# Performance work log

Measured on AMD Instinct MI355X. Metric: run time of the kernel, lower is better.

Reference implementation:

```python
import jax, jax.numpy as jnp
import numpy as np

N_NODES = 50000
N_EDGES = 800000
N_GRAPHS = 64
D_IN = 768
D_HID = 256


def gcn_conv(x, src, dst, W, b, n_nodes):
    """PyG GCNConv: symmetric-normalized aggregation with self-loops.
    out = D^{-1/2} (A + I) D^{-1/2} (x @ W) + b
    """
    h = x @ W  # [N, C_out]
    # degree from target nodes, counting the implicit self-loop (+1)
    deg = jax.ops.segment_sum(jnp.ones((src.shape[0],), h.dtype), dst,
                              num_segments=n_nodes) + 1.0
    dinv = jax.lax.rsqrt(deg)  # deg >= 1 always (self-loop)
    norm = (dinv[src] * dinv[dst])[:, None]  # [E, 1]
    agg = jax.ops.segment_sum(h[src] * norm, dst, num_segments=n_nodes)
    # self-loop contribution: norm_ii = dinv_i^2
    agg = agg + (dinv * dinv)[:, None] * h
    return agg + b


def global_mean_pool(x, batch, n_graphs):
    s = jax.ops.segment_sum(x, batch, num_segments=n_graphs)
    cnt = jax.ops.segment_sum(jnp.ones((x.shape[0],), x.dtype), batch,
                              num_segments=n_graphs)
    return s / jnp.maximum(cnt, 1.0)[:, None]


def setup_inputs() -> dict:
    key = jax.random.key(0)
    ks = jax.random.split(key, 12)
    x = jax.random.normal(ks[0], (N_NODES, D_IN), jnp.float32)
    edge_index = jax.random.randint(ks[1], (2, N_EDGES), 0, N_NODES, jnp.int64)
    batch = jnp.sort(jax.random.randint(ks[2], (N_NODES,), 0, N_GRAPHS, jnp.int64))
    def glorot(k, shape):
        lim = np.sqrt(6.0 / (shape[0] + shape[1]))
        return jax.random.uniform(k, shape, jnp.float32, -lim, lim)
    return {
        "x": x, "edge_index": edge_index, "batch": batch,
        "W1": glorot(ks[3], (D_IN, D_HID)), "b1": jnp.zeros((D_HID,), jnp.float32),
        "W2": glorot(ks[4], (D_HID, D_HID)), "b2": jnp.zeros((D_HID,), jnp.float32),
        "W3": glorot(ks[5], (D_HID, D_HID)), "b3": jnp.zeros((D_HID,), jnp.float32),
        "Wl": glorot(ks[6], (D_HID, D_IN)), "bl": jnp.zeros((D_IN,), jnp.float32),
    }


def reference(x, edge_index, batch, W1, b1, W2, b2, W3, b3, Wl, bl):
    src, dst = edge_index[0], edge_index[1]
    n = x.shape[0]
    # dropout is identity in eval mode
    h = jax.nn.relu(gcn_conv(x, src, dst, W1, b1, n))
    h = jax.nn.relu(gcn_conv(h, src, dst, W2, b2, n))
    h = gcn_conv(h, src, dst, W3, b3, n)
    g = global_mean_pool(h, batch, N_GRAPHS)  # [G, D_HID]
    return g @ Wl + bl  # [G, D_IN]
```

## Files before the change

kernel.cpp:

```cpp
#include <hip/hip_runtime.h>
#include <hip/hip_bf16.h>

#define D_IN 768
#define D_HID 256

typedef __attribute__((ext_vector_type(8))) short short8;
typedef __attribute__((ext_vector_type(4))) float f32x4;

__device__ inline float b2f(unsigned short u) {
    unsigned x = ((unsigned)u) << 16;
    union { unsigned u; float f; } c; c.u = x; return c.f;
}
__device__ inline unsigned short f2b(float v) {
    __hip_bfloat16 h = __float2bfloat16(v);
    return *(unsigned short*)&h;
}

__device__ inline void gload_lds16(const void* g, void* l) {
    __builtin_amdgcn_global_load_lds(
        (const __attribute__((address_space(1))) unsigned int*)g,
        (__attribute__((address_space(3))) unsigned int*)l, 16, 0, 0);
}


__global__ void k_count(const int* __restrict__ dst, int* __restrict__ deg, int E) {
    int i = blockIdx.x * 256 + threadIdx.x;
    if (i < E) atomicAdd(&deg[dst[i]], 1);
}

__global__ void k_dinv(const int* __restrict__ deg, float* __restrict__ dinv, int N) {
    int i = blockIdx.x * 256 + threadIdx.x;
    if (i < N) dinv[i] = rsqrtf((float)deg[i] + 1.0f);
}

__global__ __launch_bounds__(1024) void k_scan(const int* __restrict__ deg,
                                               int* __restrict__ row_ptr, int N) {
    __shared__ int wsum[16];
    __shared__ int carry_s;
    int t = threadIdx.x;
    int lane = t & 63, wid = t >> 6;
    if (t == 0) carry_s = 0;
    __syncthreads();
    for (int base = 0; base < N; base += 1024) {
        int i = base + t;
        int v = (i < N) ? deg[i] : 0;
        int s = v;
        #pragma unroll
        for (int d = 1; d < 64; d <<= 1) {
            int tmp = __shfl_up(s, d);
            if (lane >= d) s += tmp;
        }
        if (lane == 63) wsum[wid] = s;
        __syncthreads();
        if (wid == 0 && lane < 16) {
            int ws = wsum[lane];
            #pragma unroll
            for (int d = 1; d < 16; d <<= 1) {
                int tmp = __shfl_up(ws, d);
                if (lane >= d) ws += tmp;
            }
            wsum[lane] = ws;
        }
        __syncthreads();
        int carry = carry_s;
        int woff = (wid > 0) ? wsum[wid - 1] : 0;
        if (i < N) row_ptr[i] = carry + woff + s - v;
        __syncthreads();
        if (t == 0) carry_s = carry + wsum[15];
        __syncthreads();
    }
    if (t == 0) row_ptr[N] = carry_s;
}

__global__ void k_fill(const int* __restrict__ src, const int* __restrict__ dst,
                       const int* __restrict__ row_ptr, int* __restrict__ wptr,
                       int* __restrict__ csr_src, int E) {
    int i = blockIdx.x * 256 + threadIdx.x;
    if (i < E) {
        int d = dst[i];
        int w = atomicAdd(&wptr[d], 1);
        csr_src[row_ptr[d] + w] = src[i];
    }
}

__global__ void k_bounds(const int* __restrict__ batch, int* __restrict__ cnt,
                         int* __restrict__ offg, int N, int G) {
    int g = threadIdx.x;
    if (g >= G) return;
    auto lower = [&](int key) {
        int lo = 0, hi = N;
        while (lo < hi) {
            int mid = (lo + hi) >> 1;
            if (batch[mid] < key) lo = mid + 1; else hi = mid;
        }
        return lo;
    };
    int lo = lower(g);
    int hi = lower(g + 1);
    offg[g] = lo;
    cnt[g] = hi - lo;
}

__global__ void k_prep_B(const float* __restrict__ W, short* __restrict__ Bp, int KA) {
    int t = blockIdx.x * 256 + threadIdx.x;
    if (t >= KA * 256) return;
    int k = t >> 8, n = t & 255;
    float v = W[(size_t)k * 256 + n];
    unsigned short h = f2b(v);
    unsigned short l = f2b(v - b2f(h));
    int c = k >> 5, q = (k >> 3) & 3, j = k & 7;
    int tile = n >> 4, ln = n & 15;
    size_t base = (size_t)c * 16384 + (size_t)(tile * 4 + q) * 128 + ln * 8 + j;
    Bp[base] = (short)h;
    Bp[base + 8192] = (short)l;
}

template <int MODE>
__global__ __launch_bounds__(512, 4) void k_gemm4(const void* __restrict__ Av,
                                                  const short* __restrict__ Bp,
                                                  unsigned short* __restrict__ C,
                                                  int M) {
    constexpr int KA = (MODE == 1) ? D_IN : D_HID;
    constexpr int NCH = KA / 32;
    __shared__ short Bs[2][16384];

    int t = threadIdx.x;
    int lane = t & 63, w = t >> 6;
    int wr = w >> 2, wc = w & 3;
    int ln = lane & 15, q = lane >> 4;
    int bm = blockIdx.x * 128;

    const char* Abase[4];
    #pragma unroll
    for (int s = 0; s < 4; ++s) {
        int rr = bm + wr * 64 + s * 16 + ln;
        rr = (rr < M) ? rr : (M - 1);
        Abase[s] = (const char*)Av + (size_t)rr * KA * ((MODE == 1) ? 4 : 2);
    }

    f32x4 acc[4][4];
    #pragma unroll
    for (int s = 0; s < 4; ++s)
        #pragma unroll
        for (int tt = 0; tt < 4; ++tt) acc[s][tt] = (f32x4){0.f, 0.f, 0.f, 0.f};

    auto stage = [&](int c, int pb) {
        #pragma unroll
        for (int i = 0; i < 4; ++i) {
            int seg = i * 8 + w;
            gload_lds16(Bp + (size_t)c * 16384 + seg * 512 + lane * 8,
                        &Bs[pb][seg * 512]);
        }
    };

    stage(0, 0);
    __syncthreads();

    for (int c = 0; c < NCH; ++c) {
        int pb = c & 1;
        if (c + 1 < NCH) stage(c + 1, pb ^ 1);

        short8 a_hi[4], a_lo[4];
        #pragma unroll
        for (int s = 0; s < 4; ++s) {
            if (MODE == 1) {
                const float* Af = (const float*)(Abase[s]) + c * 32 + q * 8;
                f32x4 v0 = *(const f32x4*)Af;
                f32x4 v1 = *(const f32x4*)(Af + 4);
                float vv[8] = {v0[0], v0[1], v0[2], v0[3], v1[0], v1[1], v1[2], v1[3]};
                #pragma unroll
                for (int j = 0; j < 8; ++j) {
                    unsigned short h = f2b(vv[j]);
                    a_hi[s][j] = (short)h;
                    a_lo[s][j] = (short)f2b(vv[j] - b2f(h));
                }
            } else {
                const unsigned short* Ab = (const unsigned short*)(Abase[s]) + c * 32 + q * 8;
                a_hi[s] = *(const short8*)Ab;
            }
        }

        #pragma unroll
        for (int tt = 0; tt < 4; ++tt) {
            int T = wc * 4 + tt;
            const short* bp = &Bs[pb][(size_t)(T * 4 + q) * 128 + ln * 8];
            short8 bh = *(const short8*)bp;
            short8 bl = *(const short8*)(bp + 8192);
            #pragma unroll
            for (int s = 0; s < 4; ++s) {
                acc[s][tt] = __builtin_amdgcn_mfma_f32_16x16x32_bf16(a_hi[s], bh, acc[s][tt], 0, 0, 0);
                if (MODE == 1)
                    acc[s][tt] = __builtin_amdgcn_mfma_f32_16x16x32_bf16(a_lo[s], bh, acc[s][tt], 0, 0, 0);
                acc[s][tt] = __builtin_amdgcn_mfma_f32_16x16x32_bf16(
                    (MODE == 1) ? a_hi[s] : a_hi[s], bl, acc[s][tt], 0, 0, 0);
            }
        }
        __syncthreads();
    }

    #pragma unroll
    for (int s = 0; s < 4; ++s)
        #pragma unroll
        for (int tt = 0; tt < 4; ++tt)
            #pragma unroll
            for (int r = 0; r < 4; ++r) {
                int row = bm + wr * 64 + s * 16 + q * 4 + r;
                if (row < M)
                    C[(size_t)row * 256 + wc * 64 + tt * 16 + ln] = f2b(acc[s][tt][r]);
            }
}

template <int RELU, int OUTBF>
__global__ __launch_bounds__(256) void k_agg(const unsigned short* __restrict__ hin,
                                             void* __restrict__ hout,
                                             const int* __restrict__ row_ptr,
                                             const int* __restrict__ csr_src,
                                             const float* __restrict__ dinv,
                                             const float* __restrict__ bias, int N) {
    int w = threadIdx.x >> 6;
    int lane = threadIdx.x & 63;
    int row = blockIdx.x * 4 + w;
    if (row >= N) return;
    int half = lane >> 5;
    int hl = lane & 31;
    int c8 = hl * 8;

    int2 se = *(const int2*)&row_ptr[row];
    int s = se.x, e = se.y;

    float di = dinv[row];
    short8 vs = *(const short8*)&hin[(size_t)row * 256 + c8];
    float4 bb0 = *(const float4*)&bias[c8];
    float4 bb1 = *(const float4*)&bias[c8 + 4];

    float acc[8];
    #pragma unroll
    for (int ch = 0; ch < 8; ++ch) acc[ch] = 0.f;

    int j = s;
    for (; j + 8 <= e; j += 8) {
        int u[4];
        float dv[4];
        short8 v[4];
        #pragma unroll
        for (int p = 0; p < 4; ++p) {
            int2 uu = *(const int2*)&csr_src[j + 2 * p];
            u[p] = half ? uu.y : uu.x;
        }
        #pragma unroll
        for (int p = 0; p < 4; ++p) dv[p] = dinv[u[p]];
        #pragma unroll
        for (int p = 0; p < 4; ++p) v[p] = *(const short8*)&hin[(size_t)u[p] * 256 + c8];
        #pragma unroll
        for (int p = 0; p < 4; ++p)
            #pragma unroll
            for (int ch = 0; ch < 8; ++ch)
                acc[ch] += dv[p] * b2f((unsigned short)v[p][ch]);
    }
    for (; j + 2 <= e; j += 2) {
        int2 uu = *(const int2*)&csr_src[j];
        int u = half ? uu.y : uu.x;
        float dv = dinv[u];
        short8 v = *(const short8*)&hin[(size_t)u * 256 + c8];
        #pragma unroll
        for (int ch = 0; ch < 8; ++ch) acc[ch] += dv * b2f((unsigned short)v[ch]);
    }
    if (j < e) {
        int u = csr_src[j];
        float dv = half ? 0.f : dinv[u];
        short8 v = *(const short8*)&hin[(size_t)u * 256 + c8];
        #pragma unroll
        for (int ch = 0; ch < 8; ++ch) acc[ch] += dv * b2f((unsigned short)v[ch]);
    }

    #pragma unroll
    for (int ch = 0; ch < 8; ++ch) acc[ch] += __shfl_xor(acc[ch], 32);

    float dii = di * di;
    float r[8];
    #pragma unroll
    for (int ch = 0; ch < 8; ++ch) {
        float b = (ch < 4) ? ((ch == 0) ? bb0.x : (ch == 1) ? bb0.y : (ch == 2) ? bb0.z : bb0.w)
                           : ((ch == 4) ? bb1.x : (ch == 5) ? bb1.y : (ch == 6) ? bb1.z : bb1.w);
        r[ch] = acc[ch] * di + dii * b2f((unsigned short)vs[ch]) + b;
        if (RELU) r[ch] = fmaxf(r[ch], 0.f);
    }

    float r0 = half ? r[4] : r[0];
    float r1 = half ? r[5] : r[1];
    float r2 = half ? r[6] : r[2];
    float r3 = half ? r[7] : r[3];
    int cofs = c8 + half * 4;

    if (OUTBF) {
        ushort4 o;
        o.x = f2b(r0); o.y = f2b(r1); o.z = f2b(r2); o.w = f2b(r3);
        *(ushort4*)((unsigned short*)hout + (size_t)row * 256 + cofs) = o;
    } else {
        *(float4*)((float*)hout + (size_t)row * 256 + cofs) = make_float4(r0, r1, r2, r3);
    }
}

__global__ __launch_bounds__(256) void k_pool(const float* __restrict__ h,
                                              const int* __restrict__ cnt,
                                              const int* __restrict__ offg,
                                              float* __restrict__ g) {
    int gi = blockIdx.x, slice = blockIdx.y;
    int c = threadIdx.x;
    int start = offg[gi], n = cnt[gi];
    int per = (n + (int)gridDim.y - 1) / (int)gridDim.y;
    int r0 = slice * per;
    int r1 = min(n, r0 + per);
    float acc = 0.f;
    for (int r = r0; r < r1; ++r) acc += h[(size_t)(start + r) * D_HID + c];
    if (r1 > r0) atomicAdd(&g[gi * D_HID + c], acc);
}

__global__ __launch_bounds__(256) void k_final(const float* __restrict__ g,
                                               const int* __restrict__ cnt,
                                               const float* __restrict__ Wl,
                                               const float* __restrict__ bl,
                                               float* __restrict__ out) {
    __shared__ float gs[D_HID];
    int t = threadIdx.x;
    int gi = blockIdx.y;
    int c = blockIdx.x * 256 + t;
    float inv = 1.0f / (float)max(cnt[gi], 1);
    gs[t] = g[gi * D_HID + t] * inv;
    __syncthreads();
    float acc = bl[c];
    #pragma unroll 8
    for (int k = 0; k < D_HID; ++k) acc = fmaf(gs[k], Wl[(size_t)k * D_IN + c], acc);
    out[(size_t)gi * D_IN + c] = acc;
}


extern "C" void kernel_launch(void* const* d_in, const int* in_sizes, int n_in,
                              void* d_out, int out_size, void* d_ws, size_t ws_size,
                              hipStream_t stream) {
    const float* x     = (const float*)d_in[0];
    const int*   ei    = (const int*)d_in[1];
    const int*   batch = (const int*)d_in[2];
    const float* W1 = (const float*)d_in[3];
    const float* b1 = (const float*)d_in[4];
    const float* W2 = (const float*)d_in[5];
    const float* b2 = (const float*)d_in[6];
    const float* W3 = (const float*)d_in[7];
    const float* b3 = (const float*)d_in[8];
    const float* Wl = (const float*)d_in[9];
    const float* bl = (const float*)d_in[10];
    float* out = (float*)d_out;

    int N = in_sizes[2];
    int E = in_sizes[1] / 2;
    int G = out_size / D_IN;
    const int* srcp = ei;
    const int* dstp = ei + E;

    char* ws = (char*)d_ws;
    size_t o = 0;
    auto alloc = [&](size_t bytes) -> char* {
        char* p = ws + o;
        o += (bytes + 255) & ~(size_t)255;
        return p;
    };
    int*   deg     = (int*)alloc((size_t)N * 4);
    int*   wptr    = (int*)alloc((size_t)N * 4);
    int*   row_ptr = (int*)alloc((size_t)(N + 1) * 4);
    int*   cnt     = (int*)alloc((size_t)G * 4);
    int*   offg    = (int*)alloc((size_t)G * 4);
    int*   csr_src = (int*)alloc((size_t)E * 4);
    float* dinv    = (float*)alloc((size_t)N * 4);
    float* gbuf    = (float*)alloc((size_t)G * D_HID * 4);
    unsigned short* hG  = (unsigned short*)alloc((size_t)N * D_HID * 2);
    unsigned short* hA2 = (unsigned short*)alloc((size_t)N * D_HID * 2);
    float* hF      = (float*)alloc((size_t)N * D_HID * 4);
    short* Bp1     = (short*)alloc((size_t)(D_IN / 32) * 16384 * 2);
    short* Bp2     = (short*)alloc((size_t)(D_HID / 32) * 16384 * 2);
    short* Bp3     = (short*)alloc((size_t)(D_HID / 32) * 16384 * 2);

    hipMemsetAsync(deg, 0, (size_t)N * 4, stream);
    hipMemsetAsync(wptr, 0, (size_t)N * 4, stream);
    hipMemsetAsync(gbuf, 0, (size_t)G * D_HID * 4, stream);

    int gE = (E + 255) / 256;
    int gN = (N + 255) / 256;

    k_count<<<gE, 256, 0, stream>>>(dstp, deg, E);
    k_dinv<<<gN, 256, 0, stream>>>(deg, dinv, N);
    k_scan<<<1, 1024, 0, stream>>>(deg, row_ptr, N);
    k_fill<<<gE, 256, 0, stream>>>(srcp, dstp, row_ptr, wptr, csr_src, E);
    k_bounds<<<1, 64, 0, stream>>>(batch, cnt, offg, N, G);

    k_prep_B<<<D_IN, 256, 0, stream>>>(W1, Bp1, D_IN);
    k_prep_B<<<D_HID, 256, 0, stream>>>(W2, Bp2, D_HID);
    k_prep_B<<<D_HID, 256, 0, stream>>>(W3, Bp3, D_HID);

    int gemm_grid = (N + 127) / 128;
    int agg_grid = (N + 3) / 4;

    k_gemm4<1><<<gemm_grid, 512, 0, stream>>>(x, Bp1, hG, N);
    k_agg<1, 1><<<agg_grid, 256, 0, stream>>>(hG, hA2, row_ptr, csr_src, dinv, b1, N);
    k_gemm4<2><<<gemm_grid, 512, 0, stream>>>(hA2, Bp2, hG, N);
    k_agg<1, 1><<<agg_grid, 256, 0, stream>>>(hG, hA2, row_ptr, csr_src, dinv, b2, N);
    k_gemm4<2><<<gemm_grid, 512, 0, stream>>>(hA2, Bp3, hG, N);
    k_agg<0, 0><<<agg_grid, 256, 0, stream>>>(hG, hF, row_ptr, csr_src, dinv, b3, N);

    dim3 pool_grid(G, 8);
    k_pool<<<pool_grid, 256, 0, stream>>>(hF, cnt, offg, gbuf);
    dim3 fin_grid(D_IN / 256, G);
    k_final<<<fin_grid, 256, 0, stream>>>(gbuf, cnt, Wl, bl, out);
}
```

Before: 745.5 us.

## Fold last GCN layer and mean pool into a pooled weight matrix

Uses linearity: mean_pool(Â·h2·W3 + b3) = (P·Â)·h2·W3 + b3, where the pooling matrix P·Â is built as a sparse N×64 weight via edge atomics. The third GEMM, the third aggregation and the fp32 pool are replaced by a dense pool-GEMM over h2 (N×256 times N×64) followed by a tiny 64×256×256 GEMM with W3. This removes a full-size GEMM and a full gather pass over the edges. In exchange it adds a 12.8MB memset, 800k scattered atomics, and a reduction with a K dimension of 50k that has modest parallelism.

```diff
diff --git a/kernel.cpp b/kernel.cpp
--- a/kernel.cpp
+++ b/kernel.cpp
@@ -84,7 +84,8 @@
 }
 
 __global__ void k_bounds(const int* __restrict__ batch, int* __restrict__ cnt,
-                         int* __restrict__ offg, int N, int G) {
+                         int* __restrict__ offg, float* __restrict__ invc,
+                         int N, int G) {
     int g = threadIdx.x;
     if (g >= G) return;
     auto lower = [&](int key) {
@@ -99,6 +100,27 @@
     int hi = lower(g + 1);
     offg[g] = lo;
     cnt[g] = hi - lo;
+    invc[g] = 1.0f / (float)max(hi - lo, 1);
+}
+
+__global__ void k_wpool(const int* __restrict__ src, const int* __restrict__ dst,
+                        const int* __restrict__ batch, const float* __restrict__ dinv,
+                        const float* __restrict__ invc, float* __restrict__ WpT, int E) {
+    int i = blockIdx.x * 256 + threadIdx.x;
+    if (i < E) {
+        int d = dst[i], s = src[i];
+        int g = batch[d];
+        atomicAdd(&WpT[(size_t)s * 64 + g], dinv[d] * dinv[s] * invc[g]);
+    }
+}
+
+__global__ void k_wpool_self(const int* __restrict__ batch, const float* __restrict__ dinv,
+                             const float* __restrict__ invc, float* __restrict__ WpT, int N) {
+    int j = blockIdx.x * 256 + threadIdx.x;
+    if (j < N) {
+        int g = batch[j];
+        atomicAdd(&WpT[(size_t)j * 64 + g], dinv[j] * dinv[j] * invc[g]);
+    }
 }
 
 __global__ void k_prep_B(const float* __restrict__ W, short* __restrict__ Bp, int KA) {
@@ -301,23 +323,55 @@
     }
 }
 
-__global__ __launch_bounds__(256) void k_pool(const float* __restrict__ h,
-                                              const int* __restrict__ cnt,
-                                              const int* __restrict__ offg,
-                                              float* __restrict__ g) {
-    int gi = blockIdx.x, slice = blockIdx.y;
+__global__ __launch_bounds__(256) void k_poolgemm(const unsigned short* __restrict__ h,
+                                                  const float* __restrict__ WpT,
+                                                  float* __restrict__ gbuf,
+                                                  int N, int KS) {
+    int nt = blockIdx.x;
+    int ks = blockIdx.y;
+    int t = threadIdx.x;
+    int c = nt * 64 + (t & 63);
+    int gq = t >> 6;
+    int per = (N + KS - 1) / KS;
+    int j0 = ks * per;
+    int j1 = min(N, j0 + per);
+    float acc[16];
+    #pragma unroll
+    for (int i = 0; i < 16; ++i) acc[i] = 0.f;
+    for (int j = j0; j < j1; ++j) {
+        float hv = b2f(h[(size_t)j * 256 + c]);
+        const float4* wp = (const float4*)&WpT[(size_t)j * 64 + gq * 16];
+        float4 w0 = wp[0], w1 = wp[1], w2 = wp[2], w3 = wp[3];
+        acc[0]  = fmaf(w0.x, hv, acc[0]);  acc[1]  = fmaf(w0.y, hv, acc[1]);
+        acc[2]  = fmaf(w0.z, hv, acc[2]);  acc[3]  = fmaf(w0.w, hv, acc[3]);
+        acc[4]  = fmaf(w1.x, hv, acc[4]);  acc[5]  = fmaf(w1.y, hv, acc[5]);
+        acc[6]  = fmaf(w1.z, hv, acc[6]);  acc[7]  = fmaf(w1.w, hv, acc[7]);
+        acc[8]  = fmaf(w2.x, hv, acc[8]);  acc[9]  = fmaf(w2.y, hv, acc[9]);
+        acc[10] = fmaf(w2.z, hv, acc[10]); acc[11] = fmaf(w2.w, hv, acc[11]);
+        acc[12] = fmaf(w3.x, hv, acc[12]); acc[13] = fmaf(w3.y, hv, acc[13]);
+        acc[14] = fmaf(w3.z, hv, acc[14]); acc[15] = fmaf(w3.w, hv, acc[15]);
+    }
+    #pragma unroll
+    for (int i = 0; i < 16; ++i)
+        atomicAdd(&gbuf[(size_t)(gq * 16 + i) * 256 + c], acc[i]);
+}
+
+__global__ __launch_bounds__(256) void k_gW3(const float* __restrict__ gbuf,
+                                             const float* __restrict__ W3,
+                                             const float* __restrict__ b3,
+                                             float* __restrict__ gm) {
+    __shared__ float gs[D_HID];
+    int gi = blockIdx.x;
     int c = threadIdx.x;
-    int start = offg[gi], n = cnt[gi];
-    int per = (n + (int)gridDim.y - 1) / (int)gridDim.y;
-    int r0 = slice * per;
-    int r1 = min(n, r0 + per);
-    float acc = 0.f;
-    for (int r = r0; r < r1; ++r) acc += h[(size_t)(start + r) * D_HID + c];
-    if (r1 > r0) atomicAdd(&g[gi * D_HID + c], acc);
-}
-
-__global__ __launch_bounds__(256) void k_final(const float* __restrict__ g,
-                                               const int* __restrict__ cnt,
+    gs[c] = gbuf[(size_t)gi * D_HID + c];
+    __syncthreads();
+    float acc = b3[c];
+    #pragma unroll 8
+    for (int k = 0; k < D_HID; ++k) acc = fmaf(gs[k], W3[(size_t)k * D_HID + c], acc);
+    gm[(size_t)gi * D_HID + c] = acc;
+}
+
+__global__ __launch_bounds__(256) void k_final(const float* __restrict__ gm,
                                                const float* __restrict__ Wl,
                                                const float* __restrict__ bl,
                                                float* __restrict__ out) {
@@ -325,8 +379,7 @@
     int t = threadIdx.x;
     int gi = blockIdx.y;
     int c = blockIdx.x * 256 + t;
-    float inv = 1.0f / (float)max(cnt[gi], 1);
-    gs[t] = g[gi * D_HID + t] * inv;
+    gs[t] = gm[(size_t)gi * D_HID + t];
     __syncthreads();
     float acc = bl[c];
     #pragma unroll 8
@@ -369,19 +422,21 @@
     int*   row_ptr = (int*)alloc((size_t)(N + 1) * 4);
     int*   cnt     = (int*)alloc((size_t)G * 4);
     int*   offg    = (int*)alloc((size_t)G * 4);
+    float* invc    = (float*)alloc((size_t)G * 4);
     int*   csr_src = (int*)alloc((size_t)E * 4);
     float* dinv    = (float*)alloc((size_t)N * 4);
     float* gbuf    = (float*)alloc((size_t)G * D_HID * 4);
+    float* gm      = (float*)alloc((size_t)G * D_HID * 4);
     unsigned short* hG  = (unsigned short*)alloc((size_t)N * D_HID * 2);
     unsigned short* hA2 = (unsigned short*)alloc((size_t)N * D_HID * 2);
-    float* hF      = (float*)alloc((size_t)N * D_HID * 4);
+    float* WpT     = (float*)alloc((size_t)N * 64 * 4);
     short* Bp1     = (short*)alloc((size_t)(D_IN / 32) * 16384 * 2);
     short* Bp2     = (short*)alloc((size_t)(D_HID / 32) * 16384 * 2);
-    short* Bp3     = (short*)alloc((size_t)(D_HID / 32) * 16384 * 2);
 
     hipMemsetAsync(deg, 0, (size_t)N * 4, stream);
     hipMemsetAsync(wptr, 0, (size_t)N * 4, stream);
     hipMemsetAsync(gbuf, 0, (size_t)G * D_HID * 4, stream);
+    hipMemsetAsync(WpT, 0, (size_t)N * 64 * 4, stream);
 
     int gE = (E + 255) / 256;
     int gN = (N + 255) / 256;
@@ -390,11 +445,13 @@
     k_dinv<<<gN, 256, 0, stream>>>(deg, dinv, N);
     k_scan<<<1, 1024, 0, stream>>>(deg, row_ptr, N);
     k_fill<<<gE, 256, 0, stream>>>(srcp, dstp, row_ptr, wptr, csr_src, E);
-    k_bounds<<<1, 64, 0, stream>>>(batch, cnt, offg, N, G);
+    k_bounds<<<1, 64, 0, stream>>>(batch, cnt, offg, invc, N, G);
+
+    k_wpool<<<gE, 256, 0, stream>>>(srcp, dstp, batch, dinv, invc, WpT, E);
+    k_wpool_self<<<gN, 256, 0, stream>>>(batch, dinv, invc, WpT, N);
 
     k_prep_B<<<D_IN, 256, 0, stream>>>(W1, Bp1, D_IN);
     k_prep_B<<<D_HID, 256, 0, stream>>>(W2, Bp2, D_HID);
-    k_prep_B<<<D_HID, 256, 0, stream>>>(W3, Bp3, D_HID);
 
     int gemm_grid = (N + 127) / 128;
     int agg_grid = (N + 3) / 4;
@@ -403,11 +460,10 @@
     k_agg<1, 1><<<agg_grid, 256, 0, stream>>>(hG, hA2, row_ptr, csr_src, dinv, b1, N);
     k_gemm4<2><<<gemm_grid, 512, 0, stream>>>(hA2, Bp2, hG, N);
     k_agg<1, 1><<<agg_grid, 256, 0, stream>>>(hG, hA2, row_ptr, csr_src, dinv, b2, N);
-    k_gemm4<2><<<gemm_grid, 512, 0, stream>>>(hA2, Bp3, hG, N);
-    k_agg<0, 0><<<agg_grid, 256, 0, stream>>>(hG, hF, row_ptr, csr_src, dinv, b3, N);
-
-    dim3 pool_grid(G, 8);
-    k_pool<<<pool_grid, 256, 0, stream>>>(hF, cnt, offg, gbuf);
+    dim3 pg_grid(4, 128);
+    k_poolgemm<<<pg_grid, 256, 0, stream>>>(hA2, WpT, gbuf, N, 128);
+    k_gW3<<<G, 256, 0, stream>>>(gbuf, W3, b3, gm);
+
     dim3 fin_grid(D_IN / 256, G);
-    k_final<<<fin_grid, 256, 0, stream>>>(gbuf, cnt, Wl, bl, out);
-}
+    k_final<<<fin_grid, 256, 0, stream>>>(gm, Wl, bl, out);
+}
```

Result: slower. 824.4 us (+10.6%).

## Fold third GCN weight into final linear layer and retile GEMM with A-prefetch

Applied to the files above, without the earlier changes.

Layer 3's weight and the final linear layer are linear and commute with aggregation and mean pooling, so W3·Wl and b3·Wl+bl are precomputed into a combined matrix and bias. The third GEMM over all nodes is dropped, and the last aggregation runs directly on layer-2 output with a zero bias. The GEMM tile shrinks from 128 to 64 rows per block, and A fragments for the next K-chunk are register-prefetched to overlap global loads with MFMA work. The fold changes floating-point summation order. The smaller tile doubles the grid and raises B staging traffic per row.

```diff
diff --git a/kernel.cpp b/kernel.cpp
--- a/kernel.cpp
+++ b/kernel.cpp
@@ -101,6 +101,44 @@
     cnt[g] = hi - lo;
 }
 
+__global__ __launch_bounds__(256) void k_wc(const float* __restrict__ W3,
+                                            const float* __restrict__ Wl,
+                                            float* __restrict__ Wc) {
+    __shared__ float w3s[16][256];
+    int t = threadIdx.x;
+    int cx = blockIdx.x, iq = blockIdx.y;
+    #pragma unroll
+    for (int r = 0; r < 16; ++r)
+        w3s[r][t] = W3[(size_t)(iq * 16 + r) * 256 + t];
+    __syncthreads();
+    int c = cx * 256 + t;
+    float acc[16];
+    #pragma unroll
+    for (int i = 0; i < 16; ++i) acc[i] = 0.f;
+    for (int m = 0; m < 256; ++m) {
+        float wl = Wl[(size_t)m * 768 + c];
+        #pragma unroll
+        for (int i = 0; i < 16; ++i) acc[i] = fmaf(w3s[i][m], wl, acc[i]);
+    }
+    #pragma unroll
+    for (int i = 0; i < 16; ++i)
+        Wc[(size_t)(iq * 16 + i) * 768 + c] = acc[i];
+}
+
+__global__ __launch_bounds__(256) void k_bc(const float* __restrict__ b3,
+                                            const float* __restrict__ Wl,
+                                            const float* __restrict__ bl,
+                                            float* __restrict__ bc) {
+    __shared__ float b3s[256];
+    int t = threadIdx.x;
+    b3s[t] = b3[t];
+    __syncthreads();
+    int c = blockIdx.x * 256 + t;
+    float acc = bl[c];
+    for (int m = 0; m < 256; ++m) acc = fmaf(b3s[m], Wl[(size_t)m * 768 + c], acc);
+    bc[c] = acc;
+}
+
 __global__ void k_prep_B(const float* __restrict__ W, short* __restrict__ Bp, int KA) {
     int t = blockIdx.x * 256 + threadIdx.x;
     if (t >= KA * 256) return;
@@ -116,7 +154,7 @@
 }
 
 template <int MODE>
-__global__ __launch_bounds__(512, 4) void k_gemm4(const void* __restrict__ Av,
+__global__ __launch_bounds__(512, 4) void k_gemm6(const void* __restrict__ Av,
                                                   const short* __restrict__ Bp,
                                                   unsigned short* __restrict__ C,
                                                   int M) {
@@ -128,19 +166,19 @@
     int lane = t & 63, w = t >> 6;
     int wr = w >> 2, wc = w & 3;
     int ln = lane & 15, q = lane >> 4;
-    int bm = blockIdx.x * 128;
-
-    const char* Abase[4];
-    #pragma unroll
-    for (int s = 0; s < 4; ++s) {
-        int rr = bm + wr * 64 + s * 16 + ln;
+    int bm = blockIdx.x * 64;
+
+    const char* Abase[2];
+    #pragma unroll
+    for (int s = 0; s < 2; ++s) {
+        int rr = bm + wr * 32 + s * 16 + ln;
         rr = (rr < M) ? rr : (M - 1);
         Abase[s] = (const char*)Av + (size_t)rr * KA * ((MODE == 1) ? 4 : 2);
     }
 
-    f32x4 acc[4][4];
-    #pragma unroll
-    for (int s = 0; s < 4; ++s)
+    f32x4 acc[2][4];
+    #pragma unroll
+    for (int s = 0; s < 2; ++s)
         #pragma unroll
         for (int tt = 0; tt < 4; ++tt) acc[s][tt] = (f32x4){0.f, 0.f, 0.f, 0.f};
 
@@ -154,20 +192,47 @@
     };
 
     stage(0, 0);
+
+    f32x4 cur0[2], cur1[2];
+    short8 curb[2];
+    #pragma unroll
+    for (int s = 0; s < 2; ++s) {
+        if (MODE == 1) {
+            const float* Af = (const float*)(Abase[s]) + q * 8;
+            cur0[s] = *(const f32x4*)Af;
+            cur1[s] = *(const f32x4*)(Af + 4);
+        } else {
+            curb[s] = *(const short8*)((const unsigned short*)(Abase[s]) + q * 8);
+        }
+    }
     __syncthreads();
 
     for (int c = 0; c < NCH; ++c) {
         int pb = c & 1;
-        if (c + 1 < NCH) stage(c + 1, pb ^ 1);
-
-        short8 a_hi[4], a_lo[4];
-        #pragma unroll
-        for (int s = 0; s < 4; ++s) {
+        bool more = (c + 1 < NCH);
+        if (more) stage(c + 1, pb ^ 1);
+
+        f32x4 nxt0[2], nxt1[2];
+        short8 nxtb[2];
+        if (more) {
+            #pragma unroll
+            for (int s = 0; s < 2; ++s) {
+                if (MODE == 1) {
+                    const float* Af = (const float*)(Abase[s]) + (c + 1) * 32 + q * 8;
+                    nxt0[s] = *(const f32x4*)Af;
+                    nxt1[s] = *(const f32x4*)(Af + 4);
+                } else {
+                    nxtb[s] = *(const short8*)((const unsigned short*)(Abase[s]) + (c + 1) * 32 + q * 8);
+                }
+            }
+        }
+
+        short8 a_hi[2], a_lo[2];
+        #pragma unroll
+        for (int s = 0; s < 2; ++s) {
             if (MODE == 1) {
-                const float* Af = (const float*)(Abase[s]) + c * 32 + q * 8;
-                f32x4 v0 = *(const f32x4*)Af;
-                f32x4 v1 = *(const f32x4*)(Af + 4);
-                float vv[8] = {v0[0], v0[1], v0[2], v0[3], v1[0], v1[1], v1[2], v1[3]};
+                float vv[8] = {cur0[s][0], cur0[s][1], cur0[s][2], cur0[s][3],
+                               cur1[s][0], cur1[s][1], cur1[s][2], cur1[s][3]};
                 #pragma unroll
                 for (int j = 0; j < 8; ++j) {
                     unsigned short h = f2b(vv[j]);
@@ -175,8 +240,7 @@
                     a_lo[s][j] = (short)f2b(vv[j] - b2f(h));
                 }
             } else {
-                const unsigned short* Ab = (const unsigned short*)(Abase[s]) + c * 32 + q * 8;
-                a_hi[s] = *(const short8*)Ab;
+                a_hi[s] = curb[s];
             }
         }
 
@@ -185,26 +249,33 @@
             int T = wc * 4 + tt;
             const short* bp = &Bs[pb][(size_t)(T * 4 + q) * 128 + ln * 8];
             short8 bh = *(const short8*)bp;
-            short8 bl = *(const short8*)(bp + 8192);
-            #pragma unroll
-            for (int s = 0; s < 4; ++s) {
+            short8 bl2 = *(const short8*)(bp + 8192);
+            #pragma unroll
+            for (int s = 0; s < 2; ++s) {
                 acc[s][tt] = __builtin_amdgcn_mfma_f32_16x16x32_bf16(a_hi[s], bh, acc[s][tt], 0, 0, 0);
                 if (MODE == 1)
                     acc[s][tt] = __builtin_amdgcn_mfma_f32_16x16x32_bf16(a_lo[s], bh, acc[s][tt], 0, 0, 0);
-                acc[s][tt] = __builtin_amdgcn_mfma_f32_16x16x32_bf16(
-                    (MODE == 1) ? a_hi[s] : a_hi[s], bl, acc[s][tt], 0, 0, 0);
+                acc[s][tt] = __builtin_amdgcn_mfma_f32_16x16x32_bf16(a_hi[s], bl2, acc[s][tt], 0, 0, 0);
             }
         }
         __syncthreads();
-    }
-
-    #pragma unroll
-    for (int s = 0; s < 4; ++s)
+
+        if (more) {
+            #pragma unroll
+            for (int s = 0; s < 2; ++s) {
+                if (MODE == 1) { cur0[s] = nxt0[s]; cur1[s] = nxt1[s]; }
+                else           { curb[s] = nxtb[s]; }
+            }
+        }
+    }
+
+    #pragma unroll
+    for (int s = 0; s < 2; ++s)
         #pragma unroll
         for (int tt = 0; tt < 4; ++tt)
             #pragma unroll
             for (int r = 0; r < 4; ++r) {
-                int row = bm + wr * 64 + s * 16 + q * 4 + r;
+                int row = bm + wr * 32 + s * 16 + q * 4 + r;
                 if (row < M)
                     C[(size_t)row * 256 + wc * 64 + tt * 16 + ln] = f2b(acc[s][tt][r]);
             }
@@ -318,8 +389,8 @@
 
 __global__ __launch_bounds__(256) void k_final(const float* __restrict__ g,
                                                const int* __restrict__ cnt,
-                                               const float* __restrict__ Wl,
-                                               const float* __restrict__ bl,
+                                               const float* __restrict__ Wc,
+                                               const float* __restrict__ bc,
                                                float* __restrict__ out) {
     __shared__ float gs[D_HID];
     int t = threadIdx.x;
@@ -328,9 +399,9 @@
     float inv = 1.0f / (float)max(cnt[gi], 1);
     gs[t] = g[gi * D_HID + t] * inv;
     __syncthreads();
-    float acc = bl[c];
+    float acc = bc[c];
     #pragma unroll 8
-    for (int k = 0; k < D_HID; ++k) acc = fmaf(gs[k], Wl[(size_t)k * D_IN + c], acc);
+    for (int k = 0; k < D_HID; ++k) acc = fmaf(gs[k], Wc[(size_t)k * D_IN + c], acc);
     out[(size_t)gi * D_IN + c] = acc;
 }
 
@@ -372,16 +443,19 @@
     int*   csr_src = (int*)alloc((size_t)E * 4);
     float* dinv    = (float*)alloc((size_t)N * 4);
     float* gbuf    = (float*)alloc((size_t)G * D_HID * 4);
+    float* zbias   = (float*)alloc((size_t)D_HID * 4);
+    float* Wc      = (float*)alloc((size_t)D_HID * D_IN * 4);
+    float* bc      = (float*)alloc((size_t)D_IN * 4);
     unsigned short* hG  = (unsigned short*)alloc((size_t)N * D_HID * 2);
     unsigned short* hA2 = (unsigned short*)alloc((size_t)N * D_HID * 2);
     float* hF      = (float*)alloc((size_t)N * D_HID * 4);
     short* Bp1     = (short*)alloc((size_t)(D_IN / 32) * 16384 * 2);
     short* Bp2     = (short*)alloc((size_t)(D_HID / 32) * 16384 * 2);
-    short* Bp3     = (short*)alloc((size_t)(D_HID / 32) * 16384 * 2);
 
     hipMemsetAsync(deg, 0, (size_t)N * 4, stream);
     hipMemsetAsync(wptr, 0, (size_t)N * 4, stream);
     hipMemsetAsync(gbuf, 0, (size_t)G * D_HID * 4, stream);
+    hipMemsetAsync(zbias, 0, (size_t)D_HID * 4, stream);
 
     int gE = (E + 255) / 256;
     int gN = (N + 255) / 256;
@@ -394,20 +468,21 @@
 
     k_prep_B<<<D_IN, 256, 0, stream>>>(W1, Bp1, D_IN);
     k_prep_B<<<D_HID, 256, 0, stream>>>(W2, Bp2, D_HID);
-    k_prep_B<<<D_HID, 256, 0, stream>>>(W3, Bp3, D_HID);
-
-    int gemm_grid = (N + 127) / 128;
+    dim3 wc_grid(3, 16);
+    k_wc<<<wc_grid, 256, 0, stream>>>(W3, Wl, Wc);
+    k_bc<<<3, 256, 0, stream>>>(b3, Wl, bl, bc);
+
+    int gemm_grid = (N + 63) / 64;
     int agg_grid = (N + 3) / 4;
 
-    k_gemm4<1><<<gemm_grid, 512, 0, stream>>>(x, Bp1, hG, N);
+    k_gemm6<1><<<gemm_grid, 512, 0, stream>>>(x, Bp1, hG, N);
     k_agg<1, 1><<<agg_grid, 256, 0, stream>>>(hG, hA2, row_ptr, csr_src, dinv, b1, N);
-    k_gemm4<2><<<gemm_grid, 512, 0, stream>>>(hA2, Bp2, hG, N);
+    k_gemm6<2><<<gemm_grid, 512, 0, stream>>>(hA2, Bp2, hG, N);
     k_agg<1, 1><<<agg_grid, 256, 0, stream>>>(hG, hA2, row_ptr, csr_src, dinv, b2, N);
-    k_gemm4<2><<<gemm_grid, 512, 0, stream>>>(hA2, Bp3, hG, N);
-    k_agg<0, 0><<<agg_grid, 256, 0, stream>>>(hG, hF, row_ptr, csr_src, dinv, b3, N);
+    k_agg<0, 0><<<agg_grid, 256, 0, stream>>>(hA2, hF, row_ptr, csr_src, dinv, zbias, N);
 
     dim3 pool_grid(G, 8);
     k_pool<<<pool_grid, 256, 0, stream>>>(hF, cnt, offg, gbuf);
     dim3 fin_grid(D_IN / 256, G);
-    k_final<<<fin_grid, 256, 0, stream>>>(gbuf, cnt, Wl, bl, out);
-}
+    k_final<<<fin_grid, 256, 0, stream>>>(gbuf, cnt, Wc, bc, out);
+}
```

Result: slower. 765.0 us (+2.6%).

## Fold third-layer weight into final linear to skip one node GEMM

Applied to the files above, without the earlier changes.

Exploits linearity of the last GCN layer, aggregation, and mean pooling to precompute Wc = W3·Wl and bc = b3·Wl + bl. The third node-level GEMM over all nodes is removed, and the last aggregation operates on the layer-2 activations with zero bias. This trades a large N×256×256 GEMM for a tiny weight-product kernel. It changes the rounding order and shifts the bias term for graphs with zero nodes.

```diff
diff --git a/kernel.cpp b/kernel.cpp
--- a/kernel.cpp
+++ b/kernel.cpp
@@ -99,6 +99,44 @@
     int hi = lower(g + 1);
     offg[g] = lo;
     cnt[g] = hi - lo;
+}
+
+__global__ __launch_bounds__(256) void k_wc(const float* __restrict__ W3,
+                                            const float* __restrict__ Wl,
+                                            float* __restrict__ Wc) {
+    __shared__ float w3s[16][256];
+    int t = threadIdx.x;
+    int cx = blockIdx.x, iq = blockIdx.y;
+    #pragma unroll
+    for (int r = 0; r < 16; ++r)
+        w3s[r][t] = W3[(size_t)(iq * 16 + r) * 256 + t];
+    __syncthreads();
+    int c = cx * 256 + t;
+    float acc[16];
+    #pragma unroll
+    for (int i = 0; i < 16; ++i) acc[i] = 0.f;
+    for (int m = 0; m < 256; ++m) {
+        float wl = Wl[(size_t)m * 768 + c];
+        #pragma unroll
+        for (int i = 0; i < 16; ++i) acc[i] = fmaf(w3s[i][m], wl, acc[i]);
+    }
+    #pragma unroll
+    for (int i = 0; i < 16; ++i)
+        Wc[(size_t)(iq * 16 + i) * 768 + c] = acc[i];
+}
+
+__global__ __launch_bounds__(256) void k_bc(const float* __restrict__ b3,
+                                            const float* __restrict__ Wl,
+                                            const float* __restrict__ bl,
+                                            float* __restrict__ bc) {
+    __shared__ float b3s[256];
+    int t = threadIdx.x;
+    b3s[t] = b3[t];
+    __syncthreads();
+    int c = blockIdx.x * 256 + t;
+    float acc = bl[c];
+    for (int m = 0; m < 256; ++m) acc = fmaf(b3s[m], Wl[(size_t)m * 768 + c], acc);
+    bc[c] = acc;
 }
 
 __global__ void k_prep_B(const float* __restrict__ W, short* __restrict__ Bp, int KA) {
@@ -318,8 +356,8 @@
 
 __global__ __launch_bounds__(256) void k_final(const float* __restrict__ g,
                                                const int* __restrict__ cnt,
-                                               const float* __restrict__ Wl,
-                                               const float* __restrict__ bl,
+                                               const float* __restrict__ Wc,
+                                               const float* __restrict__ bc,
                                                float* __restrict__ out) {
     __shared__ float gs[D_HID];
     int t = threadIdx.x;
@@ -328,9 +366,9 @@
     float inv = 1.0f / (float)max(cnt[gi], 1);
     gs[t] = g[gi * D_HID + t] * inv;
     __syncthreads();
-    float acc = bl[c];
+    float acc = bc[c];
     #pragma unroll 8
-    for (int k = 0; k < D_HID; ++k) acc = fmaf(gs[k], Wl[(size_t)k * D_IN + c], acc);
+    for (int k = 0; k < D_HID; ++k) acc = fmaf(gs[k], Wc[(size_t)k * D_IN + c], acc);
     out[(size_t)gi * D_IN + c] = acc;
 }
 
@@ -372,16 +410,19 @@
     int*   csr_src = (int*)alloc((size_t)E * 4);
     float* dinv    = (float*)alloc((size_t)N * 4);
     float* gbuf    = (float*)alloc((size_t)G * D_HID * 4);
+    float* zbias   = (float*)alloc((size_t)D_HID * 4);
+    float* Wc      = (float*)alloc((size_t)D_HID * D_IN * 4);
+    float* bc      = (float*)alloc((size_t)D_IN * 4);
     unsigned short* hG  = (unsigned short*)alloc((size_t)N * D_HID * 2);
     unsigned short* hA2 = (unsigned short*)alloc((size_t)N * D_HID * 2);
     float* hF      = (float*)alloc((size_t)N * D_HID * 4);
     short* Bp1     = (short*)alloc((size_t)(D_IN / 32) * 16384 * 2);
     short* Bp2     = (short*)alloc((size_t)(D_HID / 32) * 16384 * 2);
-    short* Bp3     = (short*)alloc((size_t)(D_HID / 32) * 16384 * 2);
 
     hipMemsetAsync(deg, 0, (size_t)N * 4, stream);
     hipMemsetAsync(wptr, 0, (size_t)N * 4, stream);
     hipMemsetAsync(gbuf, 0, (size_t)G * D_HID * 4, stream);
+    hipMemsetAsync(zbias, 0, (size_t)D_HID * 4, stream);
 
     int gE = (E + 255) / 256;
     int gN = (N + 255) / 256;
@@ -394,7 +435,9 @@
 
     k_prep_B<<<D_IN, 256, 0, stream>>>(W1, Bp1, D_IN);
     k_prep_B<<<D_HID, 256, 0, stream>>>(W2, Bp2, D_HID);
-    k_prep_B<<<D_HID, 256, 0, stream>>>(W3, Bp3, D_HID);
+    dim3 wc_grid(3, 16);
+    k_wc<<<wc_grid, 256, 0, stream>>>(W3, Wl, Wc);
+    k_bc<<<3, 256, 0, stream>>>(b3, Wl, bl, bc);
 
     int gemm_grid = (N + 127) / 128;
     int agg_grid = (N + 3) / 4;
@@ -403,11 +446,10 @@
     k_agg<1, 1><<<agg_grid, 256, 0, stream>>>(hG, hA2, row_ptr, csr_src, dinv, b1, N);
     k_gemm4<2><<<gemm_grid, 512, 0, stream>>>(hA2, Bp2, hG, N);
     k_agg<1, 1><<<agg_grid, 256, 0, stream>>>(hG, hA2, row_ptr, csr_src, dinv, b2, N);
-    k_gemm4<2><<<gemm_grid, 512, 0, stream>>>(hA2, Bp3, hG, N);
-    k_agg<0, 0><<<agg_grid, 256, 0, stream>>>(hG, hF, row_ptr, csr_src, dinv, b3, N);
+    k_agg<0, 0><<<agg_grid, 256, 0, stream>>>(hA2, hF, row_ptr, csr_src, dinv, zbias, N);
 
     dim3 pool_grid(G, 8);
     k_pool<<<pool_grid, 256, 0, stream>>>(hF, cnt, offg, gbuf);
     dim3 fin_grid(D_IN / 256, G);
-    k_final<<<fin_grid, 256, 0, stream>>>(gbuf, cnt, Wl, bl, out);
-}
+    k_final<<<fin_grid, 256, 0, stream>>>(gbuf, cnt, Wc, bc, out);
+}
```

Result: no change. 750.5 us (+0.7%).
